# Performance work log

Hardware: AMD Instinct MI355X
Metric: run time of the kernel (lower is better)

The kernel has to match this reference:

```python
import jax, jax.numpy as jnp
import numpy as np

E = 8           # num experts
TOPK = 2
NUM_TOKENS = 4096
K = 2048        # hidden dim
N = 2816        # intermediate dim
P = NUM_TOKENS * TOPK   # num_valid_tokens (token, expert-slot) pairs
PE = P // E             # pairs per expert (token-sorted, equal load)


def setup_inputs() -> dict:
    key = jax.random.key(0)
    ks = jax.random.split(key, 6)
    x = jax.random.normal(ks[0], (NUM_TOKENS, K), dtype=jnp.float32)
    W1 = jax.random.normal(ks[1], (E, N, K), dtype=jnp.float32) * (K ** -0.5)  # gate proj
    W3 = jax.random.normal(ks[2], (E, N, K), dtype=jnp.float32) * (K ** -0.5)  # up proj
    W2 = jax.random.normal(ks[3], (E, K, N), dtype=jnp.float32) * (N ** -0.5)  # down proj
    topk_weights = jax.random.uniform(ks[4], (P,), dtype=jnp.float32)          # router weights per pair
    sorted_token_ids = jax.random.randint(ks[5], (P,), 0, NUM_TOKENS, dtype=jnp.int32)
    # token-sorted dispatch: pairs grouped by expert, equal count per expert
    expert_ids = jnp.repeat(jnp.arange(E, dtype=jnp.int32), PE)
    return {"x": x, "W1": W1, "W3": W3, "W2": W2,
            "topk_weights": topk_weights,
            "sorted_token_ids": sorted_token_ids,
            "expert_ids": expert_ids}


def reference(x, W1, W3, W2, topk_weights, sorted_token_ids, expert_ids):
    # Pairs are grouped by expert (token-sorted dispatch), PE pairs per expert.
    eids = expert_ids.reshape(E, PE)[:, 0]            # expert id per group
    xg = x[sorted_token_ids].reshape(E, PE, K)        # gather token activations per pair
    gate = jnp.einsum('epk,enk->epn', xg, W1[eids])   # [E, PE, N]
    up = jnp.einsum('epk,enk->epn', xg, W3[eids])     # [E, PE, N]
    # kernel computes sigmoid(gate) * up (as written in the triton body)
    h = jax.nn.sigmoid(gate) * up
    out_p = jnp.einsum('epn,ekn->epk', h, W2[eids])   # down proj, [E, PE, K]
    out_p = out_p * topk_weights.reshape(E, PE, 1)
    # scatter-add per-pair results into per-token output (atomic_add in kernel)
    out = jnp.zeros((x.shape[0], K), dtype=x.dtype)
    out = out.at[sorted_token_ids].add(out_p.reshape(P, K))
    return out
```

## Files before the change

kernel.cpp:

```cpp
#include <hip/hip_runtime.h>
#include <hip/hip_bf16.h>
#include <cstdint>

typedef __bf16 bf16_t;
typedef __attribute__((ext_vector_type(8))) __bf16 bf16x8;
typedef __attribute__((ext_vector_type(4))) __bf16 bf16x4;
typedef __attribute__((ext_vector_type(4))) float f32x4;

#define NEXP 8
#define DK   2048
#define DN   2816
#define DN2  5632
#define NP   8192
#define PPE  1024

__global__ void k_cvt_w13(const float* __restrict__ W1, const float* __restrict__ W3,
                          bf16_t* __restrict__ dst) {
    const int total4 = NEXP * DN * (DK / 4);
    int stride = gridDim.x * blockDim.x;
    for (int i = blockIdx.x * blockDim.x + threadIdx.x; i < 2 * total4; i += stride) {
        int sel = i >= total4;
        int j   = sel ? i - total4 : i;
        int g   = j >> 9;
        int c4  = j & 511;
        int e   = g / DN;
        int n   = g - e * DN;
        long drow = (long)e * DN2 + ((n >> 4) << 5) + (n & 15) + (sel ? 16 : 0);
        float4 v = reinterpret_cast<const float4*>(sel ? W3 : W1)[j];
        bf16x4 o = { (bf16_t)v.x, (bf16_t)v.y, (bf16_t)v.z, (bf16_t)v.w };
        *reinterpret_cast<bf16x4*>(dst + drow * DK + c4 * 4) = o;
    }
}

__global__ void k_cvt(const float* __restrict__ src, bf16_t* __restrict__ dst, int total4) {
    int stride = gridDim.x * blockDim.x;
    for (int i = blockIdx.x * blockDim.x + threadIdx.x; i < total4; i += stride) {
        float4 v = reinterpret_cast<const float4*>(src)[i];
        bf16x4 o = { (bf16_t)v.x, (bf16_t)v.y, (bf16_t)v.z, (bf16_t)v.w };
        reinterpret_cast<bf16x4*>(dst)[i] = o;
    }
}

__global__ void k_gather(const float* __restrict__ x, const int* __restrict__ ids,
                         bf16_t* __restrict__ xg) {
    int i = blockIdx.x * blockDim.x + threadIdx.x;
    if (i >= NP * (DK / 4)) return;
    int p  = i >> 9;
    int c4 = i & 511;
    int tok = ids[p];
    float4 v = reinterpret_cast<const float4*>(x + (size_t)tok * DK)[c4];
    bf16x4 o = { (bf16_t)v.x, (bf16_t)v.y, (bf16_t)v.z, (bf16_t)v.w };
    *reinterpret_cast<bf16x4*>(xg + (size_t)p * DK + c4 * 4) = o;
}

__device__ __forceinline__ void gl2lds16(const bf16_t* g, bf16_t* l) {
    __builtin_amdgcn_global_load_lds(
        (__attribute__((address_space(1))) void*)(const_cast<bf16_t*>(g)),
        (__attribute__((address_space(3))) void*)(l), 16, 0, 0);
}

#define BARX()  __builtin_amdgcn_s_barrier()
#define LGKM0() asm volatile("s_waitcnt lgkmcnt(0)" ::: "memory")
#define LGKM8() asm volatile("s_waitcnt lgkmcnt(8)" ::: "memory")
#define VMW6()  asm volatile("s_waitcnt vmcnt(6)" ::: "memory")
#define VMW0()  asm volatile("s_waitcnt vmcnt(0)" ::: "memory")

#define STG(ARR, SRC, LD, BUF, HALF, KT) do {                                   \
    gl2lds16((SRC) + (long)((HALF) * 128) * (LD) + (long)(KT) * 64,             \
             &ARR[BUF][(HALF) * 128 + w8][0]);                                  \
    gl2lds16((SRC) + (long)((HALF) * 128 + 64) * (LD) + (long)(KT) * 64,        \
             &ARR[BUF][(HALF) * 128 + 64 + w8][0]);                             \
} while (0)

#define LOADA(DST, BASE) do { _Pragma("unroll")                                 \
    for (int mi_ = 0; mi_ < 4; ++mi_) {                                         \
        DST[mi_][0] = *reinterpret_cast<const bf16x8*>((BASE) + aoff0 + mi_ * 1024); \
        DST[mi_][1] = *reinterpret_cast<const bf16x8*>((BASE) + aoff1 + mi_ * 1024); \
    } } while (0)

#define LOADB(DST, BASE) do { _Pragma("unroll")                                 \
    for (int ni_ = 0; ni_ < 2; ++ni_) {                                         \
        DST[ni_][0] = *reinterpret_cast<const bf16x8*>((BASE) + boff0 + ni_ * 1024); \
        DST[ni_][1] = *reinterpret_cast<const bf16x8*>((BASE) + boff1 + ni_ * 1024); \
    } } while (0)

#define MFMAQ(AF, BF, MIB, NIB) do {                                            \
    __builtin_amdgcn_s_setprio(1);                                              \
    _Pragma("unroll") for (int kk_ = 0; kk_ < 2; ++kk_)                         \
    _Pragma("unroll") for (int mi_ = 0; mi_ < 4; ++mi_)                         \
    _Pragma("unroll") for (int ni_ = 0; ni_ < 2; ++ni_)                         \
        acc[(MIB) + mi_][(NIB) + ni_] = __builtin_amdgcn_mfma_f32_16x16x32_bf16( \
            AF[mi_][kk_], BF[ni_][kk_], acc[(MIB) + mi_][(NIB) + ni_], 0, 0, 0); \
    __builtin_amdgcn_s_setprio(0);                                              \
} while (0)

template <int EPI>
__launch_bounds__(512, 2)
__global__ void k_gemm(const bf16_t* __restrict__ A, const bf16_t* __restrict__ B,
                       bf16_t* __restrict__ Hout, float* __restrict__ Fout,
                       const float* __restrict__ tw, const int* __restrict__ ids,
                       int Mtiles, int Ntiles, int nkt, int lda, int ldb,
                       long aStride, long bStride) {
    __shared__ bf16_t As[2][256][64];
    __shared__ bf16_t Bs[2][256][64];

    const int nwg = gridDim.x;
    const int logical = (blockIdx.x & 7) * (nwg >> 3) + (blockIdx.x >> 3);
    const int tpe = Mtiles * Ntiles;
    const int e  = logical / tpe;
    const int r  = logical - e * tpe;
    const int nt = r / Mtiles;
    const int mt = r - nt * Mtiles;

    const int tid  = threadIdx.x;
    const int w    = tid >> 6;
    const int w8   = w * 8;
    const int lane = tid & 63;
    const int wr = w >> 2, wc = w & 3;
    const int fr = lane & 15;
    const int fc = lane >> 4;

    const int srow = tid >> 3;
    const int schk = (tid & 7) ^ (srow & 7);
    const bf16_t* aSrc = A + (long)e * aStride + ((long)mt * 256 + srow) * lda + schk * 8;
    const bf16_t* bSrc = B + (long)e * bStride + ((long)nt * 256 + srow) * ldb + schk * 8;

    const int sx = lane & 7;
    const int aoff0 = (wr * 128 + fr) * 64 + ((0 + fc) ^ sx) * 8;
    const int aoff1 = (wr * 128 + fr) * 64 + ((4 + fc) ^ sx) * 8;
    const int boff0 = (wc * 64 + fr) * 64 + ((0 + fc) ^ sx) * 8;
    const int boff1 = (wc * 64 + fr) * 64 + ((4 + fc) ^ sx) * 8;

    const bf16_t* As0 = &As[0][0][0];
    const bf16_t* As1 = &As[1][0][0];
    const bf16_t* Bs0 = &Bs[0][0][0];
    const bf16_t* Bs1 = &Bs[1][0][0];

    f32x4 acc[8][4];
#pragma unroll
    for (int a = 0; a < 8; ++a)
#pragma unroll
        for (int b = 0; b < 4; ++b) acc[a][b] = (f32x4){0.f, 0.f, 0.f, 0.f};

    bf16x8 af[4][2], ah[4][2], bl[2][2], bh[2][2];

    STG(Bs, bSrc, ldb, 0, 0, 0); STG(Bs, bSrc, ldb, 0, 1, 0);
    STG(As, aSrc, lda, 0, 0, 0); STG(As, aSrc, lda, 0, 1, 0);
    STG(Bs, bSrc, ldb, 1, 0, 1); STG(Bs, bSrc, ldb, 1, 1, 1);
    STG(As, aSrc, lda, 1, 0, 1);
    VMW6();
    BARX();

    const int nIter = nkt >> 1;
    for (int it = 0; it < nIter; ++it) {
        const int t = it * 2;
        const bool last = (it == nIter - 1);
        LOADA(af, As0); LOADB(bl, Bs0);
        STG(As, aSrc, lda, 1, 1, t + 1);
        LGKM8();
        BARX(); LGKM0();
        MFMAQ(af, bl, 0, 0);
        BARX();
        LOADB(bh, Bs0 + 2048);
        BARX(); LGKM0();
        MFMAQ(af, bh, 0, 2);
        BARX();
        LOADA(ah, As0 + 4096);
        if (!last) { STG(Bs, bSrc, ldb, 0, 0, t + 2); STG(Bs, bSrc, ldb, 0, 1, t + 2); }
        BARX(); LGKM0();
        MFMAQ(ah, bh, 4, 2);
        BARX();
        if (!last) { STG(As, aSrc, lda, 0, 0, t + 2); VMW6(); } else { VMW0(); }
        BARX();
        MFMAQ(ah, bl, 4, 0);
        BARX();
        LOADA(af, As1); LOADB(bl, Bs1);
        if (!last) STG(As, aSrc, lda, 0, 1, t + 2);
        LGKM8();
        BARX(); LGKM0();
        MFMAQ(af, bl, 0, 0);
        BARX();
        LOADB(bh, Bs1 + 2048);
        BARX(); LGKM0();
        MFMAQ(af, bh, 0, 2);
        BARX();
        LOADA(ah, As1 + 4096);
        if (!last) { STG(Bs, bSrc, ldb, 1, 0, t + 3); STG(Bs, bSrc, ldb, 1, 1, t + 3); }
        BARX(); LGKM0();
        MFMAQ(ah, bh, 4, 2);
        BARX();
        if (!last) { STG(As, aSrc, lda, 1, 0, t + 3); VMW6(); } else { VMW0(); }
        BARX();
        MFMAQ(ah, bl, 4, 0);
        BARX();
    }

    if constexpr (EPI == 0) {
        const long prow0 = (long)e * PPE + (long)mt * 256 + wr * 128 + fc * 4;
        const int col0 = nt * 128 + wc * 32 + fr;
#pragma unroll
        for (int mi = 0; mi < 8; ++mi)
#pragma unroll
            for (int i = 0; i < 4; ++i) {
                long row = prow0 + mi * 16 + i;
#pragma unroll
                for (int p = 0; p < 2; ++p) {
                    float g = acc[mi][2 * p][i];
                    float u = acc[mi][2 * p + 1][i];
                    float s = 1.f / (1.f + __expf(-g));
                    Hout[row * DN + col0 + p * 16] = (bf16_t)(s * u);
                }
            }
    } else {
        const int p0 = e * PPE + mt * 256 + wr * 128 + fc * 4;
        const int col0 = nt * 256 + wc * 64 + fr;
#pragma unroll
        for (int mi = 0; mi < 8; ++mi)
#pragma unroll
            for (int i = 0; i < 4; ++i) {
                int gp = p0 + mi * 16 + i;
                float wgt = tw[gp];
                float* ob = Fout + (long)ids[gp] * DK + col0;
#pragma unroll
                for (int ni = 0; ni < 4; ++ni)
                    atomicAdd(ob + ni * 16, acc[mi][ni][i] * wgt);
            }
    }
}

extern "C" void kernel_launch(void* const* d_in, const int* in_sizes, int n_in,
                              void* d_out, int out_size, void* d_ws, size_t ws_size,
                              hipStream_t stream) {
    const float* x   = (const float*)d_in[0];
    const float* W1  = (const float*)d_in[1];
    const float* W3  = (const float*)d_in[2];
    const float* W2  = (const float*)d_in[3];
    const float* tw  = (const float*)d_in[4];
    const int*   sid = (const int*)d_in[5];
    float* out = (float*)d_out;

    char* ws = (char*)d_ws;
    bf16_t* w13i = (bf16_t*)ws;
    bf16_t* w2b  = (bf16_t*)(ws + 184549376L);
    bf16_t* xg   = (bf16_t*)(ws + 276824064L);
    bf16_t* h    = (bf16_t*)(ws + 310378496L);

    hipMemsetAsync(d_out, 0, (size_t)out_size * sizeof(float), stream);

    k_cvt_w13<<<2048, 256, 0, stream>>>(W1, W3, w13i);
    k_cvt<<<2048, 256, 0, stream>>>(W2, w2b, NEXP * DK * (DN / 4));
    k_gather<<<NP * (DK / 4) / 256, 256, 0, stream>>>(x, sid, xg);

    k_gemm<0><<<NEXP * 4 * 22, 512, 0, stream>>>(
        xg, w13i, h, nullptr, nullptr, nullptr,
        4, 22, 32, DK, DK, (long)PPE * DK, (long)DN2 * DK);

    k_gemm<1><<<NEXP * 4 * 8, 512, 0, stream>>>(
        h, w2b, nullptr, out, tw, sid,
        4, 8, 44, DN, DN, (long)PPE * DN, (long)DK * DN);
}
```

Before: 521.4 us.

## Fuse fp32-to-bf16 weight conversion into GEMM B-tile loading

Removes the separate weight conversion kernels and instead loads fp32 weights directly in the GEMMs, converting to bf16 in registers before writing the swizzled LDS tile. The W1/W3 interleave is done through address computation. This drops a full read-write pass over roughly 270 MB of weights. In exchange, each GEMM reads fp32 B tiles (twice the bytes), re-reads them for every M tile, and uses register-staged loads in place of direct global-to-LDS loads, which adds VGPR pressure.

```diff
diff --git a/kernel.cpp b/kernel.cpp
--- a/kernel.cpp
+++ b/kernel.cpp
@@ -13,33 +13,6 @@
 #define DN2  5632
 #define NP   8192
 #define PPE  1024
-
-__global__ void k_cvt_w13(const float* __restrict__ W1, const float* __restrict__ W3,
-                          bf16_t* __restrict__ dst) {
-    const int total4 = NEXP * DN * (DK / 4);
-    int stride = gridDim.x * blockDim.x;
-    for (int i = blockIdx.x * blockDim.x + threadIdx.x; i < 2 * total4; i += stride) {
-        int sel = i >= total4;
-        int j   = sel ? i - total4 : i;
-        int g   = j >> 9;
-        int c4  = j & 511;
-        int e   = g / DN;
-        int n   = g - e * DN;
-        long drow = (long)e * DN2 + ((n >> 4) << 5) + (n & 15) + (sel ? 16 : 0);
-        float4 v = reinterpret_cast<const float4*>(sel ? W3 : W1)[j];
-        bf16x4 o = { (bf16_t)v.x, (bf16_t)v.y, (bf16_t)v.z, (bf16_t)v.w };
-        *reinterpret_cast<bf16x4*>(dst + drow * DK + c4 * 4) = o;
-    }
-}
-
-__global__ void k_cvt(const float* __restrict__ src, bf16_t* __restrict__ dst, int total4) {
-    int stride = gridDim.x * blockDim.x;
-    for (int i = blockIdx.x * blockDim.x + threadIdx.x; i < total4; i += stride) {
-        float4 v = reinterpret_cast<const float4*>(src)[i];
-        bf16x4 o = { (bf16_t)v.x, (bf16_t)v.y, (bf16_t)v.z, (bf16_t)v.w };
-        reinterpret_cast<bf16x4*>(dst)[i] = o;
-    }
-}
 
 __global__ void k_gather(const float* __restrict__ x, const int* __restrict__ ids,
                          bf16_t* __restrict__ xg) {
@@ -61,15 +34,30 @@
 
 #define BARX()  __builtin_amdgcn_s_barrier()
 #define LGKM0() asm volatile("s_waitcnt lgkmcnt(0)" ::: "memory")
-#define LGKM8() asm volatile("s_waitcnt lgkmcnt(8)" ::: "memory")
-#define VMW6()  asm volatile("s_waitcnt vmcnt(6)" ::: "memory")
 #define VMW0()  asm volatile("s_waitcnt vmcnt(0)" ::: "memory")
 
-#define STG(ARR, SRC, LD, BUF, HALF, KT) do {                                   \
-    gl2lds16((SRC) + (long)((HALF) * 128) * (LD) + (long)(KT) * 64,             \
-             &ARR[BUF][(HALF) * 128 + w8][0]);                                  \
-    gl2lds16((SRC) + (long)((HALF) * 128 + 64) * (LD) + (long)(KT) * 64,        \
-             &ARR[BUF][(HALF) * 128 + 64 + w8][0]);                             \
+#define STGA(BUF, HALF, KT) do {                                                \
+    gl2lds16(aSrc + (long)((HALF) * 128) * lda + (long)(KT) * 64,               \
+             &As[BUF][(HALF) * 128 + w8][0]);                                   \
+    gl2lds16(aSrc + (long)((HALF) * 128 + 64) * lda + (long)(KT) * 64,          \
+             &As[BUF][(HALF) * 128 + 64 + w8][0]);                              \
+} while (0)
+
+#define BISSUE(DST, BQ, KT) do {                                                \
+    const float* p_ = (BQ) + (long)(KT) * 64;                                   \
+    DST[0] = *reinterpret_cast<const float4*>(p_);                              \
+    DST[1] = *reinterpret_cast<const float4*>(p_ + 4);                          \
+    DST[2] = *reinterpret_cast<const float4*>(p_ + 8);                          \
+    DST[3] = *reinterpret_cast<const float4*>(p_ + 12);                         \
+} while (0)
+
+#define BWRITE(SRC, BUF, HALF) do {                                             \
+    bf16x8 lo_ = { (bf16_t)SRC[0].x, (bf16_t)SRC[0].y, (bf16_t)SRC[0].z, (bf16_t)SRC[0].w, \
+                   (bf16_t)SRC[1].x, (bf16_t)SRC[1].y, (bf16_t)SRC[1].z, (bf16_t)SRC[1].w }; \
+    bf16x8 hi_ = { (bf16_t)SRC[2].x, (bf16_t)SRC[2].y, (bf16_t)SRC[2].z, (bf16_t)SRC[2].w, \
+                   (bf16_t)SRC[3].x, (bf16_t)SRC[3].y, (bf16_t)SRC[3].z, (bf16_t)SRC[3].w }; \
+    *reinterpret_cast<bf16x8*>(&Bs[BUF][(HALF) * 128 + trow][bc0sw]) = lo_;     \
+    *reinterpret_cast<bf16x8*>(&Bs[BUF][(HALF) * 128 + trow][bc1sw]) = hi_;     \
 } while (0)
 
 #define LOADA(DST, BASE) do { _Pragma("unroll")                                 \
@@ -96,11 +84,11 @@
 
 template <int EPI>
 __launch_bounds__(512, 2)
-__global__ void k_gemm(const bf16_t* __restrict__ A, const bf16_t* __restrict__ B,
+__global__ void k_gemm(const bf16_t* __restrict__ A, const float* __restrict__ Bf1,
+                       const float* __restrict__ Bf3,
                        bf16_t* __restrict__ Hout, float* __restrict__ Fout,
                        const float* __restrict__ tw, const int* __restrict__ ids,
-                       int Mtiles, int Ntiles, int nkt, int lda, int ldb,
-                       long aStride, long bStride) {
+                       int Mtiles, int Ntiles, int nkt, int lda, long aStride) {
     __shared__ bf16_t As[2][256][64];
     __shared__ bf16_t Bs[2][256][64];
 
@@ -123,7 +111,26 @@
     const int srow = tid >> 3;
     const int schk = (tid & 7) ^ (srow & 7);
     const bf16_t* aSrc = A + (long)e * aStride + ((long)mt * 256 + srow) * lda + schk * 8;
-    const bf16_t* bSrc = B + (long)e * bStride + ((long)nt * 256 + srow) * ldb + schk * 8;
+
+    const int trow = tid >> 2;
+    const int tc0  = (tid & 3) * 2;
+    const int bsw  = trow & 7;
+    const int bc0sw = (tc0 ^ bsw) * 8;
+    const int bc1sw = ((tc0 + 1) ^ bsw) * 8;
+    const float* bQ0;
+    const float* bQ1;
+    if constexpr (EPI == 0) {
+        int n0 = nt * 256 + trow;
+        int n1 = n0 + 128;
+        int s0 = (n0 >> 4) & 1, s1 = (n1 >> 4) & 1;
+        int r0 = ((n0 >> 5) << 4) | (n0 & 15);
+        int r1 = ((n1 >> 5) << 4) | (n1 & 15);
+        bQ0 = (s0 ? Bf3 : Bf1) + ((long)e * DN + r0) * DK + tc0 * 8;
+        bQ1 = (s1 ? Bf3 : Bf1) + ((long)e * DN + r1) * DK + tc0 * 8;
+    } else {
+        bQ0 = Bf1 + (long)e * DK * DN + ((long)nt * 256 + trow) * DN + tc0 * 8;
+        bQ1 = bQ0 + 128L * DN;
+    }
 
     const int sx = lane & 7;
     const int aoff0 = (wr * 128 + fr) * 64 + ((0 + fc) ^ sx) * 8;
@@ -136,60 +143,70 @@
     const bf16_t* Bs0 = &Bs[0][0][0];
     const bf16_t* Bs1 = &Bs[1][0][0];
 
+    bf16x8 af[4][2], ah[4][2], bl[2][2], bh[2][2];
+    float4 bq[4];
+
+    {
+        float4 p0[4], p1[4], p2[4], p3[4];
+        BISSUE(p0, bQ0, 0); BISSUE(p1, bQ1, 0);
+        BISSUE(p2, bQ0, 1); BISSUE(p3, bQ1, 1);
+        STGA(0, 0, 0); STGA(0, 1, 0);
+        STGA(1, 0, 1);
+        BWRITE(p0, 0, 0); BWRITE(p1, 0, 1);
+        BWRITE(p2, 1, 0); BWRITE(p3, 1, 1);
+        VMW0(); LGKM0();
+    }
+    BARX();
+
     f32x4 acc[8][4];
 #pragma unroll
     for (int a = 0; a < 8; ++a)
 #pragma unroll
         for (int b = 0; b < 4; ++b) acc[a][b] = (f32x4){0.f, 0.f, 0.f, 0.f};
-
-    bf16x8 af[4][2], ah[4][2], bl[2][2], bh[2][2];
-
-    STG(Bs, bSrc, ldb, 0, 0, 0); STG(Bs, bSrc, ldb, 0, 1, 0);
-    STG(As, aSrc, lda, 0, 0, 0); STG(As, aSrc, lda, 0, 1, 0);
-    STG(Bs, bSrc, ldb, 1, 0, 1); STG(Bs, bSrc, ldb, 1, 1, 1);
-    STG(As, aSrc, lda, 1, 0, 1);
-    VMW6();
-    BARX();
 
     const int nIter = nkt >> 1;
     for (int it = 0; it < nIter; ++it) {
         const int t = it * 2;
         const bool last = (it == nIter - 1);
         LOADA(af, As0); LOADB(bl, Bs0);
-        STG(As, aSrc, lda, 1, 1, t + 1);
-        LGKM8();
         BARX(); LGKM0();
         MFMAQ(af, bl, 0, 0);
         BARX();
         LOADB(bh, Bs0 + 2048);
+        if (!last) BISSUE(bq, bQ0, t + 2);
+        STGA(1, 1, t + 1);
         BARX(); LGKM0();
         MFMAQ(af, bh, 0, 2);
+        if (!last) BWRITE(bq, 0, 0);
         BARX();
         LOADA(ah, As0 + 4096);
-        if (!last) { STG(Bs, bSrc, ldb, 0, 0, t + 2); STG(Bs, bSrc, ldb, 0, 1, t + 2); }
+        if (!last) BISSUE(bq, bQ1, t + 2);
         BARX(); LGKM0();
         MFMAQ(ah, bh, 4, 2);
-        BARX();
-        if (!last) { STG(As, aSrc, lda, 0, 0, t + 2); VMW6(); } else { VMW0(); }
+        if (!last) BWRITE(bq, 0, 1);
+        BARX();
+        if (!last) STGA(0, 0, t + 2); else VMW0();
         BARX();
         MFMAQ(ah, bl, 4, 0);
         BARX();
         LOADA(af, As1); LOADB(bl, Bs1);
-        if (!last) STG(As, aSrc, lda, 0, 1, t + 2);
-        LGKM8();
+        if (!last) STGA(0, 1, t + 2);
         BARX(); LGKM0();
         MFMAQ(af, bl, 0, 0);
         BARX();
         LOADB(bh, Bs1 + 2048);
+        if (!last) BISSUE(bq, bQ0, t + 3);
         BARX(); LGKM0();
         MFMAQ(af, bh, 0, 2);
+        if (!last) BWRITE(bq, 1, 0);
         BARX();
         LOADA(ah, As1 + 4096);
-        if (!last) { STG(Bs, bSrc, ldb, 1, 0, t + 3); STG(Bs, bSrc, ldb, 1, 1, t + 3); }
+        if (!last) BISSUE(bq, bQ1, t + 3);
         BARX(); LGKM0();
         MFMAQ(ah, bh, 4, 2);
-        BARX();
-        if (!last) { STG(As, aSrc, lda, 1, 0, t + 3); VMW6(); } else { VMW0(); }
+        if (!last) BWRITE(bq, 1, 1);
+        BARX();
+        if (!last) STGA(1, 0, t + 3);
         BARX();
         MFMAQ(ah, bl, 4, 0);
         BARX();
@@ -240,22 +257,17 @@
     float* out = (float*)d_out;
 
     char* ws = (char*)d_ws;
-    bf16_t* w13i = (bf16_t*)ws;
-    bf16_t* w2b  = (bf16_t*)(ws + 184549376L);
-    bf16_t* xg   = (bf16_t*)(ws + 276824064L);
-    bf16_t* h    = (bf16_t*)(ws + 310378496L);
+    bf16_t* xg = (bf16_t*)ws;
+    bf16_t* h  = (bf16_t*)(ws + 33554432L);
 
     hipMemsetAsync(d_out, 0, (size_t)out_size * sizeof(float), stream);
-
-    k_cvt_w13<<<2048, 256, 0, stream>>>(W1, W3, w13i);
-    k_cvt<<<2048, 256, 0, stream>>>(W2, w2b, NEXP * DK * (DN / 4));
     k_gather<<<NP * (DK / 4) / 256, 256, 0, stream>>>(x, sid, xg);
 
     k_gemm<0><<<NEXP * 4 * 22, 512, 0, stream>>>(
-        xg, w13i, h, nullptr, nullptr, nullptr,
-        4, 22, 32, DK, DK, (long)PPE * DK, (long)DN2 * DK);
+        xg, W1, W3, h, nullptr, nullptr, nullptr,
+        4, 22, 32, DK, (long)PPE * DK);
 
     k_gemm<1><<<NEXP * 4 * 8, 512, 0, stream>>>(
-        h, w2b, nullptr, out, tw, sid,
-        4, 8, 44, DN, DN, (long)PPE * DN, (long)DK * DN);
-}
+        h, W2, nullptr, nullptr, out, tw, sid,
+        4, 8, 44, DN, (long)PPE * DN);
+}
```

Result: slower. 541.3 us (+3.8%).

## Load B operand directly from global into registers, bypassing LDS

Applied to the files above, without the earlier changes.

Removes the shared-memory staging buffer for the B (weight) tile and has each lane load its MFMA B fragments straight from global memory into registers, double-buffered across k-steps. This halves LDS usage and drops the LDS read traffic for B, which could allow higher occupancy and shorter barrier windows. In exchange, B rows are no longer shared across warps in a workgroup row, so global/L2 traffic for weights rises. Register pressure also goes up from the extra fragment buffers, and the prefetch indices are clamped at the end of the K loop.

```diff
diff --git a/kernel.cpp b/kernel.cpp
--- a/kernel.cpp
+++ b/kernel.cpp
@@ -61,15 +61,14 @@
 
 #define BARX()  __builtin_amdgcn_s_barrier()
 #define LGKM0() asm volatile("s_waitcnt lgkmcnt(0)" ::: "memory")
-#define LGKM8() asm volatile("s_waitcnt lgkmcnt(8)" ::: "memory")
-#define VMW6()  asm volatile("s_waitcnt vmcnt(6)" ::: "memory")
+#define VMW10() asm volatile("s_waitcnt vmcnt(10)" ::: "memory")
 #define VMW0()  asm volatile("s_waitcnt vmcnt(0)" ::: "memory")
 
-#define STG(ARR, SRC, LD, BUF, HALF, KT) do {                                   \
-    gl2lds16((SRC) + (long)((HALF) * 128) * (LD) + (long)(KT) * 64,             \
-             &ARR[BUF][(HALF) * 128 + w8][0]);                                  \
-    gl2lds16((SRC) + (long)((HALF) * 128 + 64) * (LD) + (long)(KT) * 64,        \
-             &ARR[BUF][(HALF) * 128 + 64 + w8][0]);                             \
+#define STGA(BUF, HALF, KT) do {                                                \
+    gl2lds16(aSrc + (long)((HALF) * 128) * lda + (long)(KT) * 64,               \
+             &As[BUF][(HALF) * 128 + w8][0]);                                   \
+    gl2lds16(aSrc + (long)((HALF) * 128 + 64) * lda + (long)(KT) * 64,          \
+             &As[BUF][(HALF) * 128 + 64 + w8][0]);                              \
 } while (0)
 
 #define LOADA(DST, BASE) do { _Pragma("unroll")                                 \
@@ -78,10 +77,11 @@
         DST[mi_][1] = *reinterpret_cast<const bf16x8*>((BASE) + aoff1 + mi_ * 1024); \
     } } while (0)
 
-#define LOADB(DST, BASE) do { _Pragma("unroll")                                 \
-    for (int ni_ = 0; ni_ < 2; ++ni_) {                                         \
-        DST[ni_][0] = *reinterpret_cast<const bf16x8*>((BASE) + boff0 + ni_ * 1024); \
-        DST[ni_][1] = *reinterpret_cast<const bf16x8*>((BASE) + boff1 + ni_ * 1024); \
+#define BLD(DST, ROWOFF, KT) do { _Pragma("unroll")                             \
+    for (int ni_ = 0; ni_ < 2; ++ni_) { _Pragma("unroll")                       \
+        for (int kk_ = 0; kk_ < 2; ++kk_)                                       \
+            DST[ni_][kk_] = *reinterpret_cast<const bf16x8*>(                   \
+                bLane + (long)((ROWOFF) + ni_ * 16) * ldb + (long)(KT) * 64 + kk_ * 32); \
     } } while (0)
 
 #define MFMAQ(AF, BF, MIB, NIB) do {                                            \
@@ -102,7 +102,6 @@
                        int Mtiles, int Ntiles, int nkt, int lda, int ldb,
                        long aStride, long bStride) {
     __shared__ bf16_t As[2][256][64];
-    __shared__ bf16_t Bs[2][256][64];
 
     const int nwg = gridDim.x;
     const int logical = (blockIdx.x & 7) * (nwg >> 3) + (blockIdx.x >> 3);
@@ -123,18 +122,16 @@
     const int srow = tid >> 3;
     const int schk = (tid & 7) ^ (srow & 7);
     const bf16_t* aSrc = A + (long)e * aStride + ((long)mt * 256 + srow) * lda + schk * 8;
-    const bf16_t* bSrc = B + (long)e * bStride + ((long)nt * 256 + srow) * ldb + schk * 8;
+
+    const bf16_t* bLane = B + (long)e * bStride
+                        + ((long)nt * 256 + wc * 64 + fr) * ldb + fc * 8;
 
     const int sx = lane & 7;
     const int aoff0 = (wr * 128 + fr) * 64 + ((0 + fc) ^ sx) * 8;
     const int aoff1 = (wr * 128 + fr) * 64 + ((4 + fc) ^ sx) * 8;
-    const int boff0 = (wc * 64 + fr) * 64 + ((0 + fc) ^ sx) * 8;
-    const int boff1 = (wc * 64 + fr) * 64 + ((4 + fc) ^ sx) * 8;
 
     const bf16_t* As0 = &As[0][0][0];
     const bf16_t* As1 = &As[1][0][0];
-    const bf16_t* Bs0 = &Bs[0][0][0];
-    const bf16_t* Bs1 = &Bs[1][0][0];
 
     f32x4 acc[8][4];
 #pragma unroll
@@ -142,58 +139,63 @@
 #pragma unroll
         for (int b = 0; b < 4; ++b) acc[a][b] = (f32x4){0.f, 0.f, 0.f, 0.f};
 
-    bf16x8 af[4][2], ah[4][2], bl[2][2], bh[2][2];
-
-    STG(Bs, bSrc, ldb, 0, 0, 0); STG(Bs, bSrc, ldb, 0, 1, 0);
-    STG(As, aSrc, lda, 0, 0, 0); STG(As, aSrc, lda, 0, 1, 0);
-    STG(Bs, bSrc, ldb, 1, 0, 1); STG(Bs, bSrc, ldb, 1, 1, 1);
-    STG(As, aSrc, lda, 1, 0, 1);
-    VMW6();
+    bf16x8 a[4][2];
+    bf16x8 bl0[2][2], bl1[2][2], bhS[2][2];
+
+    const int last = nkt - 1;
+
+    STGA(0, 0, 0); STGA(0, 1, 0);
+    STGA(1, 0, 1);
+    BLD(bl0, 0, 0);
+    BLD(bhS, 32, 0);
+    VMW10();
     BARX();
 
     const int nIter = nkt >> 1;
     for (int it = 0; it < nIter; ++it) {
         const int t = it * 2;
-        const bool last = (it == nIter - 1);
-        LOADA(af, As0); LOADB(bl, Bs0);
-        STG(As, aSrc, lda, 1, 1, t + 1);
-        LGKM8();
-        BARX(); LGKM0();
-        MFMAQ(af, bl, 0, 0);
-        BARX();
-        LOADB(bh, Bs0 + 2048);
-        BARX(); LGKM0();
-        MFMAQ(af, bh, 0, 2);
-        BARX();
-        LOADA(ah, As0 + 4096);
-        if (!last) { STG(Bs, bSrc, ldb, 0, 0, t + 2); STG(Bs, bSrc, ldb, 0, 1, t + 2); }
-        BARX(); LGKM0();
-        MFMAQ(ah, bh, 4, 2);
-        BARX();
-        if (!last) { STG(As, aSrc, lda, 0, 0, t + 2); VMW6(); } else { VMW0(); }
-        BARX();
-        MFMAQ(ah, bl, 4, 0);
-        BARX();
-        LOADA(af, As1); LOADB(bl, Bs1);
-        if (!last) STG(As, aSrc, lda, 0, 1, t + 2);
-        LGKM8();
-        BARX(); LGKM0();
-        MFMAQ(af, bl, 0, 0);
-        BARX();
-        LOADB(bh, Bs1 + 2048);
-        BARX(); LGKM0();
-        MFMAQ(af, bh, 0, 2);
-        BARX();
-        LOADA(ah, As1 + 4096);
-        if (!last) { STG(Bs, bSrc, ldb, 1, 0, t + 3); STG(Bs, bSrc, ldb, 1, 1, t + 3); }
-        BARX(); LGKM0();
-        MFMAQ(ah, bh, 4, 2);
-        BARX();
-        if (!last) { STG(As, aSrc, lda, 1, 0, t + 3); VMW6(); } else { VMW0(); }
-        BARX();
-        MFMAQ(ah, bl, 4, 0);
-        BARX();
-    }
+        const int tc2 = t + 2 < last ? t + 2 : last;
+        const int tc3 = t + 3 < last ? t + 3 : last;
+        LOADA(a, As0);
+        STGA(1, 1, t + 1);
+        BLD(bl1, 0, t + 1);
+        BARX(); LGKM0();
+        MFMAQ(a, bl0, 0, 0);
+        BARX();
+        BARX();
+        MFMAQ(a, bhS, 0, 2);
+        BARX();
+        LOADA(a, As0 + 4096);
+        BARX(); LGKM0();
+        MFMAQ(a, bhS, 4, 2);
+        BARX();
+        STGA(0, 0, tc2);
+        BLD(bhS, 32, t + 1);
+        VMW10();
+        BARX();
+        MFMAQ(a, bl0, 4, 0);
+        BARX();
+        LOADA(a, As1);
+        STGA(0, 1, tc2);
+        BLD(bl0, 0, tc2);
+        BARX(); LGKM0();
+        MFMAQ(a, bl1, 0, 0);
+        BARX();
+        BARX();
+        MFMAQ(a, bhS, 0, 2);
+        BARX();
+        LOADA(a, As1 + 4096);
+        BARX(); LGKM0();
+        MFMAQ(a, bhS, 4, 2);
+        BARX();
+        STGA(1, 0, tc3);
+        BLD(bhS, 32, tc2);
+        VMW10();
+        BARX();
+        MFMAQ(a, bl1, 4, 0);
+        BARX();
+    }
+    VMW0(); LGKM0();
 
     if constexpr (EPI == 0) {
         const long prow0 = (long)e * PPE + (long)mt * 256 + wr * 128 + fc * 4;
```

New measurement: 687.7 us. 31.9% more time.
